# Optimization experiments

Hardware: AMD Instinct MI355X
Metric: run time of the kernel (lower is better)

## Reference

```python
import jax, jax.numpy as jnp
import numpy as np

N_CHANNELS = 32
DIM_CAPSULE = 16


def setup_inputs() -> dict:
    key = jax.random.key(0)
    k1, k2, k3 = jax.random.split(key, 3)
    B, H, W, Cin = 32, 56, 56, 256
    d, n = DIM_CAPSULE, N_CHANNELS
    inputs = jax.random.normal(k1, (B, H, W, Cin), dtype=jnp.float32)
    # glorot-ish scale for the 3x3 conv kernel
    convW_1 = jax.random.normal(k2, (3, 3, Cin, d * n), dtype=jnp.float32) * 0.02
    bias_1 = jnp.zeros((d * n,), dtype=jnp.float32)
    CapsAct_W = jax.random.normal(k3, (1, 1, d, d * n), dtype=jnp.float32) * 0.1
    CapsAct_B = jnp.zeros((d * n,), dtype=jnp.float32)
    return {"inputs": inputs, "convW_1": convW_1, "bias_1": bias_1,
            "CapsAct_W": CapsAct_W, "CapsAct_B": CapsAct_B}


def reference(inputs, convW_1, bias_1, CapsAct_W, CapsAct_B):
    d, n = DIM_CAPSULE, N_CHANNELS
    # 3x3 stride-2 SAME conv (NHWC / HWIO), bias, relu
    y = jax.lax.conv_general_dilated(
        inputs, convW_1, window_strides=(2, 2), padding="SAME",
        dimension_numbers=("NHWC", "HWIO", "NHWC"))
    y = jax.nn.relu(y + bias_1)                      # [B, Ho, Wo, d*n]
    B, Ho, Wo, _ = y.shape
    # Per-channel 1x1 convs == grouped matmul over capsule channels.
    yg = y.reshape(B, Ho, Wo, n, d)                  # group channels: [B,Ho,Wo,n,d_in]
    Wg = CapsAct_W.reshape(d, n, d)                  # [d_in, n, d_out]
    bg = CapsAct_B.reshape(n, d)                     # [n, d_out]
    # output layout matches tf: [B, Ho, Wo, dim_capsule, n_channels]
    out = jnp.einsum("bhwnd,dne->bhwen", yg, Wg) + bg.T[None, None, None]
    return out
```

## Files before the change

kernel.cpp:

```cpp
#include <hip/hip_runtime.h>
#include <hip/hip_bf16.h>

typedef __attribute__((ext_vector_type(4))) float f32x4;
typedef __attribute__((ext_vector_type(8))) short s16x8;
typedef __attribute__((ext_vector_type(8))) unsigned short u16x8;
typedef __attribute__((ext_vector_type(4))) unsigned short u16x4;

__device__ __forceinline__ unsigned short bfbits(float f) {
  unsigned int u = __builtin_bit_cast(unsigned int, f);
  return (unsigned short)((u + 0x8000u) >> 16);
}

__device__ __forceinline__ void gll16(void* lds, const void* g) {
  __builtin_amdgcn_global_load_lds(
      (const __attribute__((address_space(1))) unsigned int*)g,
      (__attribute__((address_space(3))) unsigned int*)lds, 16, 0, 0);
}

__global__ void prep_weights(const float* __restrict__ w,
                             __hip_bfloat16* __restrict__ wt) {
  int u = blockIdx.x * 256 + threadIdx.x;
  int n = u & 511;
  int c8 = (u >> 9) & 31;
  int kpos = u >> 14;
  int t = kpos * 8 + (c8 >> 2);
  int cq = c8 & 3;
  const float* src = w + ((kpos * 256 + c8 * 8) * 512) + n;
  u16x8 d;
#pragma unroll
  for (int j = 0; j < 8; ++j) d[j] = bfbits(src[j * 512]);
  int nb = n >> 7, nl = n & 127;
  *reinterpret_cast<u16x8*>(wt + ((t * 4 + nb) * 4096 + cq * 1024 + nl * 8)) = d;
}

__global__ __launch_bounds__(256)
void prep_input_t(const float* __restrict__ in, __hip_bfloat16* __restrict__ dst) {
  __shared__ __align__(16) unsigned short row[14848];
  int bh = blockIdx.x;
  int h = bh % 57, b = bh / 57;
  int t = threadIdx.x;
  __hip_bfloat16* d = (__hip_bfloat16*)dst + (long)bh * 14848;
  if (h < 56) {
    if (t < 64) {
      int par = t >> 5, cq = t & 31;
      u16x4 z = {0, 0, 0, 0};
      *(u16x4*)(row + (par * 32 + cq) * 232 + 224) = z;
      *(u16x4*)(row + (par * 32 + cq) * 232 + 228) = z;
    }
    const float* src = in + (long)(b * 56 + h) * 56 * 256;
#pragma unroll
    for (int j = 0; j < 14; ++j) {
      int idx = j * 256 + t;
      f32x4 v = *(const f32x4*)(src + idx * 4);
      int e0 = idx * 4;
      int w = e0 >> 8, c = e0 & 255;
      int off = ((w & 1) * 32 + (c >> 3)) * 232 + (w >> 1) * 8 + (c & 7);
      u16x4 q = {bfbits(v[0]), bfbits(v[1]), bfbits(v[2]), bfbits(v[3])};
      *(u16x4*)(row + off) = q;
    }
    __syncthreads();
    for (int i = t; i < 1856; i += 256)
      *(u16x8*)(d + i * 8) = *(const u16x8*)(row + i * 8);
  } else {
    u16x8 z = {0, 0, 0, 0, 0, 0, 0, 0};
    for (int i = t; i < 1856; i += 256) *(u16x8*)(d + i * 8) = z;
  }
}

__global__ __launch_bounds__(512, 4)
void caps_main_fast(const __hip_bfloat16* __restrict__ inp,
                    const __hip_bfloat16* __restrict__ wt,
                    const float* __restrict__ bias1,
                    const float* __restrict__ capsW,
                    const float* __restrict__ capsB,
                    float* __restrict__ out) {
  __shared__ __align__(16) unsigned char smem[73728];

  int bid = (int)blockIdx.x;
  bid = (bid & 7) * 49 + (bid >> 3);
  int mblk = bid >> 2;
  int nb = bid & 3;
  int p0 = mblk * 256;

  int tid = threadIdx.x;
  int lane = tid & 63;
  int wv = tid >> 6;
  int wm = (wv >> 1) * 64;
  int wn = (wv & 1) * 64;
  int col = lane & 15;
  int lq = lane >> 4;

  int mq = wv >> 1;
  int cqa = (wv & 1) * 2;
  int bcq = wv >> 1;
  int bnh = wv & 1;

  int p = p0 + mq * 64 + lane;
  int b = p / 784;
  int rr = p - b * 784;
  int ho = rr / 28;
  int wo = rr - ho * 28;
  int base0 = b * 846336 + 2 * ho * 14848 + wo * 8;

  const __hip_bfloat16* wtb = wt + nb * 4096;

  f32x4 acc[4][4] = {};

  auto stage = [&](int buf, int t) {
    int kp = t >> 3, tc = t & 7;
    int kh = (kp * 11) >> 5;
    int kw = kp - kh * 3;
    __hip_bfloat16* sa = (__hip_bfloat16*)smem + buf * 12288;
    __hip_bfloat16* sb = sa + 8192;
    const __hip_bfloat16* as =
        inp + base0 + kh * 14848 + (kw & 1) * 7424 + (kw >> 1) * 8 + (tc * 4 + cqa) * 232;
    gll16(sa + cqa * 2048 + mq * 512, as);
    gll16(sa + (cqa + 1) * 2048 + mq * 512, as + 232);
    const __hip_bfloat16* bs = wtb + t * 16384 + bcq * 1024 + bnh * 512 + lane * 8;
    gll16(sb + bcq * 1024 + bnh * 512, bs);
  };

  stage(0, 0);
  stage(1, 1);
  __asm__ volatile("s_waitcnt vmcnt(3)" ::: "memory");
  __builtin_amdgcn_s_barrier();

  int rd = 0;
  for (int t = 0; t < 72; ++t) {
    const __hip_bfloat16* sa = (const __hip_bfloat16*)smem + rd * 12288;
    const __hip_bfloat16* sb = sa + 8192;
    s16x8 af[4], bfr[4];
#pragma unroll
    for (int mf = 0; mf < 4; ++mf)
      af[mf] = *(const s16x8*)(sa + lq * 2048 + (wm + 16 * mf + col) * 8);
#pragma unroll
    for (int nf = 0; nf < 4; ++nf)
      bfr[nf] = *(const s16x8*)(sb + lq * 1024 + (wn + 16 * nf + col) * 8);
    if (t + 2 < 72) {
      int st = rd + 2; if (st >= 3) st -= 3;
      stage(st, t + 2);
    }
#pragma unroll
    for (int mf = 0; mf < 4; ++mf)
#pragma unroll
      for (int nf = 0; nf < 4; ++nf)
        acc[mf][nf] = __builtin_amdgcn_mfma_f32_16x16x32_bf16(
            af[mf], bfr[nf], acc[mf][nf], 0, 0, 0);
    if (t < 70) {
      __asm__ volatile("s_waitcnt vmcnt(3)" ::: "memory");
    } else {
      __asm__ volatile("s_waitcnt vmcnt(0)" ::: "memory");
    }
    __builtin_amdgcn_s_barrier();
    rd = (rd + 1 == 3) ? 0 : rd + 1;
  }

  __hip_bfloat16* yw = (__hip_bfloat16*)smem + wv * 4096;
  int nBase = nb * 128 + wn;
#pragma unroll
  for (int nf = 0; nf < 4; ++nf) {
    float b1v = bias1[nBase + nf * 16 + col];
#pragma unroll
    for (int mf = 0; mf < 4; ++mf) {
      f32x4 a = acc[mf][nf];
#pragma unroll
      for (int r = 0; r < 4; ++r) {
        int pl = mf * 16 + lq * 4 + r;
        int nl = nf * 16 + col;
        float v = a[r] + b1v;
        v = v > 0.f ? v : 0.f;
        int off = (pl * 128 + nl * 2) ^ ((pl & 7) << 4);
        *(unsigned short*)((char*)yw + off) = bfbits(v);
      }
    }
  }

  int gb = nb * 8 + (wv & 1) * 4;
  s16x8 wf[4];
  f32x4 cinit[4];
#pragma unroll
  for (int g = 0; g < 4; ++g) {
    int gg = gb + g;
    s16x8 bw = {0, 0, 0, 0, 0, 0, 0, 0};
    if (lq < 2) {
#pragma unroll
      for (int j = 0; j < 8; ++j)
        bw[j] = (short)bfbits(capsW[(8 * lq + j) * 512 + gg * 16 + col]);
    }
    wf[g] = bw;
    float cb = capsB[gg * 16 + col];
    cinit[g] = f32x4{cb, cb, cb, cb};
  }
#pragma unroll
  for (int mf = 0; mf < 4; ++mf) {
    int prow = 16 * mf + col;
    f32x4 dd[4];
#pragma unroll
    for (int g = 0; g < 4; ++g) {
      s16x8 afv = {0, 0, 0, 0, 0, 0, 0, 0};
      if (lq < 2) {
        int off = (prow * 128 + g * 32 + lq * 16) ^ ((prow & 7) << 4);
        afv = *(const s16x8*)((char*)yw + off);
      }
      dd[g] = __builtin_amdgcn_mfma_f32_16x16x32_bf16(afv, wf[g], cinit[g], 0, 0, 0);
    }
    long pgl = (long)(p0 + wm) + 16 * mf;
#pragma unroll
    for (int r = 0; r < 4; ++r) {
      long pg = pgl + 4 * lq + r;
      f32x4 o = {dd[0][r], dd[1][r], dd[2][r], dd[3][r]};
      *(f32x4*)(out + (pg * 16 + col) * 32 + gb) = o;
    }
  }
}

__global__ __launch_bounds__(256, 3)
void caps_main_v1(const float* __restrict__ in, const __hip_bfloat16* __restrict__ wt,
                  const float* __restrict__ bias1, const float* __restrict__ capsW,
                  const float* __restrict__ capsB, float* __restrict__ out) {
  __shared__ __align__(16) unsigned char smem[32768];
  __hip_bfloat16* sA = (__hip_bfloat16*)smem;
  __hip_bfloat16* sB = (__hip_bfloat16*)(smem + 8192);

  int bid = (int)blockIdx.x;
  bid = (bid & 7) * 98 + (bid >> 3);
  int mblk = bid >> 2;
  int nb = bid & 3;
  int p0 = mblk * 128;

  int tid = threadIdx.x;
  int lane = tid & 63;
  int wv = tid >> 6;
  int wm = (wv >> 1) * 64;
  int wn = (wv & 1) * 64;
  int col = lane & 15;
  int lq = lane >> 4;

  int am = tid & 127;
  int ah = tid >> 7;
  int p = p0 + am;
  int bb = p / 784;
  int rr = p - bb * 784;
  int ho = rr / 28;
  int wo = rr - ho * 28;

  f32x4 acc[4][4] = {};
  const __hip_bfloat16* wtb = wt + nb * 4096;

  for (int kp = 0; kp < 9; ++kp) {
    int kh = kp / 3;
    int kw = kp - kh * 3;
    int h = 2 * ho + kh, ww = 2 * wo + kw;
    bool valid = (h < 56) && (ww < 56);
    const float* arow = in + (((bb * 56 + h) * 56 + ww) * 256) + ah * 16;
#pragma unroll
    for (int tc = 0; tc < 8; ++tc) {
      int t = kp * 8 + tc;
      __syncthreads();
      const __hip_bfloat16* bsrc = wtb + t * 16384 + tid * 8;
      gll16(sB + (wv * 512), bsrc);
      gll16(sB + 2048 + (wv * 512), bsrc + 2048);
      f32x4 v0, v1, v2, v3;
      if (valid) {
        const f32x4* apv = (const f32x4*)(arow + tc * 32);
        v0 = apv[0]; v1 = apv[1]; v2 = apv[2]; v3 = apv[3];
      } else {
        v0 = f32x4{0.f, 0.f, 0.f, 0.f}; v1 = v0; v2 = v0; v3 = v0;
      }
      u16x8 pk0, pk1;
#pragma unroll
      for (int j = 0; j < 4; ++j) {
        pk0[j] = bfbits(v0[j]); pk0[j + 4] = bfbits(v1[j]);
        pk1[j] = bfbits(v2[j]); pk1[j + 4] = bfbits(v3[j]);
      }
      *(u16x8*)(sA + (ah * 2) * 1024 + am * 8) = pk0;
      *(u16x8*)(sA + (ah * 2 + 1) * 1024 + am * 8) = pk1;
      __syncthreads();
      s16x8 af[4], bfr[4];
#pragma unroll
      for (int mf = 0; mf < 4; ++mf)
        af[mf] = *(const s16x8*)(sA + lq * 1024 + (wm + 16 * mf + col) * 8);
#pragma unroll
      for (int nf = 0; nf < 4; ++nf)
        bfr[nf] = *(const s16x8*)(sB + lq * 1024 + (wn + 16 * nf + col) * 8);
#pragma unroll
      for (int mf = 0; mf < 4; ++mf)
#pragma unroll
        for (int nf = 0; nf < 4; ++nf)
          acc[mf][nf] = __builtin_amdgcn_mfma_f32_16x16x32_bf16(
              af[mf], bfr[nf], acc[mf][nf], 0, 0, 0);
    }
  }

  __syncthreads();

  __hip_bfloat16* yw = (__hip_bfloat16*)smem + wv * 4096;
  int nBase = nb * 128 + wn;
#pragma unroll
  for (int nf = 0; nf < 4; ++nf) {
    float b1v = bias1[nBase + nf * 16 + col];
#pragma unroll
    for (int mf = 0; mf < 4; ++mf) {
      f32x4 a = acc[mf][nf];
#pragma unroll
      for (int r = 0; r < 4; ++r) {
        int pl = mf * 16 + lq * 4 + r;
        int nl = nf * 16 + col;
        float v = a[r] + b1v;
        v = v > 0.f ? v : 0.f;
        int off = (pl * 128 + nl * 2) ^ ((pl & 7) << 4);
        *(unsigned short*)((char*)yw + off) = bfbits(v);
      }
    }
  }

  int gb = nb * 8 + (wv & 1) * 4;
  s16x8 wf[4];
  f32x4 cinit[4];
#pragma unroll
  for (int g = 0; g < 4; ++g) {
    int gg = gb + g;
    s16x8 bw = {0, 0, 0, 0, 0, 0, 0, 0};
    if (lq < 2) {
#pragma unroll
      for (int j = 0; j < 8; ++j)
        bw[j] = (short)bfbits(capsW[(8 * lq + j) * 512 + gg * 16 + col]);
    }
    wf[g] = bw;
    float cb = capsB[gg * 16 + col];
    cinit[g] = f32x4{cb, cb, cb, cb};
  }
#pragma unroll
  for (int mf = 0; mf < 4; ++mf) {
    int prow = 16 * mf + col;
    f32x4 dd[4];
#pragma unroll
    for (int g = 0; g < 4; ++g) {
      s16x8 afv = {0, 0, 0, 0, 0, 0, 0, 0};
      if (lq < 2) {
        int off = (prow * 128 + g * 32 + lq * 16) ^ ((prow & 7) << 4);
        afv = *(const s16x8*)((char*)yw + off);
      }
      dd[g] = __builtin_amdgcn_mfma_f32_16x16x32_bf16(afv, wf[g], cinit[g], 0, 0, 0);
    }
    long pgl = (long)(p0 + wm) + 16 * mf;
#pragma unroll
    for (int r = 0; r < 4; ++r) {
      long pg = pgl + 4 * lq + r;
      f32x4 o = {dd[0][r], dd[1][r], dd[2][r], dd[3][r]};
      *(f32x4*)(out + (pg * 16 + col) * 32 + gb) = o;
    }
  }
}

extern "C" void kernel_launch(void* const* d_in, const int* in_sizes, int n_in,
                              void* d_out, int out_size, void* d_ws, size_t ws_size,
                              hipStream_t stream) {
  const float* inputs = (const float*)d_in[0];
  const float* convW  = (const float*)d_in[1];
  const float* bias1  = (const float*)d_in[2];
  const float* capsW  = (const float*)d_in[3];
  const float* capsB  = (const float*)d_in[4];
  float* out = (float*)d_out;

  __hip_bfloat16* wt = (__hip_bfloat16*)d_ws;
  const size_t IN_OFF = 2621440;
  const size_t NEED = IN_OFF + (size_t)27082752 * 2;

  prep_weights<<<576, 256, 0, stream>>>(convW, wt);
  if (ws_size >= NEED) {
    __hip_bfloat16* inp = (__hip_bfloat16*)((char*)d_ws + IN_OFF);
    prep_input_t<<<1824, 256, 0, stream>>>(inputs, inp);
    caps_main_fast<<<392, 512, 0, stream>>>(inp, wt, bias1, capsW, capsB, out);
  } else {
    caps_main_v1<<<784, 256, 0, stream>>>(inputs, wt, bias1, capsW, capsB, out);
  }
}
```

Baseline: 109.7 us.

## Load conv A fragments directly from global and merge prep kernels

The main conv loop stops staging the input (A) tiles through LDS and has each wave read its A fragments straight from global memory into registers. Only the weight (B) tile still goes through LDS, now double-buffered, and the MFMA block is raised in priority with setprio. The two prep kernels are merged into one launch to cut launch overhead, and the LDS footprint shrinks. The risks are exposed global latency on A, because those loads are used in the same iteration without prefetch, and duplicate A loads across waves. The fallback path also writes the converted input into a workspace that is too small for it.

After: 108.9 us. Within noise of the previous version (-0.7%).

```diff
diff --git a/kernel.cpp b/kernel.cpp
--- a/kernel.cpp
+++ b/kernel.cpp
@@ -17,53 +17,53 @@
       (__attribute__((address_space(3))) unsigned int*)lds, 16, 0, 0);
 }
 
-__global__ void prep_weights(const float* __restrict__ w,
-                             __hip_bfloat16* __restrict__ wt) {
-  int u = blockIdx.x * 256 + threadIdx.x;
-  int n = u & 511;
-  int c8 = (u >> 9) & 31;
-  int kpos = u >> 14;
-  int t = kpos * 8 + (c8 >> 2);
-  int cq = c8 & 3;
-  const float* src = w + ((kpos * 256 + c8 * 8) * 512) + n;
-  u16x8 d;
-#pragma unroll
-  for (int j = 0; j < 8; ++j) d[j] = bfbits(src[j * 512]);
-  int nb = n >> 7, nl = n & 127;
-  *reinterpret_cast<u16x8*>(wt + ((t * 4 + nb) * 4096 + cq * 1024 + nl * 8)) = d;
-}
-
 __global__ __launch_bounds__(256)
-void prep_input_t(const float* __restrict__ in, __hip_bfloat16* __restrict__ dst) {
-  __shared__ __align__(16) unsigned short row[14848];
-  int bh = blockIdx.x;
-  int h = bh % 57, b = bh / 57;
+void prep_all(const float* __restrict__ in, __hip_bfloat16* __restrict__ dst,
+              const float* __restrict__ w, __hip_bfloat16* __restrict__ wt) {
   int t = threadIdx.x;
-  __hip_bfloat16* d = (__hip_bfloat16*)dst + (long)bh * 14848;
-  if (h < 56) {
-    if (t < 64) {
-      int par = t >> 5, cq = t & 31;
-      u16x4 z = {0, 0, 0, 0};
-      *(u16x4*)(row + (par * 32 + cq) * 232 + 224) = z;
-      *(u16x4*)(row + (par * 32 + cq) * 232 + 228) = z;
-    }
-    const float* src = in + (long)(b * 56 + h) * 56 * 256;
-#pragma unroll
-    for (int j = 0; j < 14; ++j) {
-      int idx = j * 256 + t;
-      f32x4 v = *(const f32x4*)(src + idx * 4);
-      int e0 = idx * 4;
-      int w = e0 >> 8, c = e0 & 255;
-      int off = ((w & 1) * 32 + (c >> 3)) * 232 + (w >> 1) * 8 + (c & 7);
-      u16x4 q = {bfbits(v[0]), bfbits(v[1]), bfbits(v[2]), bfbits(v[3])};
-      *(u16x4*)(row + off) = q;
-    }
-    __syncthreads();
-    for (int i = t; i < 1856; i += 256)
-      *(u16x8*)(d + i * 8) = *(const u16x8*)(row + i * 8);
+  if (blockIdx.x < 1824) {
+    __shared__ __align__(16) unsigned short row[14848];
+    int bh = blockIdx.x;
+    int h = bh % 57, b = bh / 57;
+    __hip_bfloat16* d = (__hip_bfloat16*)dst + (long)bh * 14848;
+    if (h < 56) {
+      if (t < 64) {
+        int par = t >> 5, cq = t & 31;
+        u16x4 z = {0, 0, 0, 0};
+        *(u16x4*)(row + (par * 32 + cq) * 232 + 224) = z;
+        *(u16x4*)(row + (par * 32 + cq) * 232 + 228) = z;
+      }
+      const float* src = in + (long)(b * 56 + h) * 56 * 256;
+#pragma unroll
+      for (int j = 0; j < 14; ++j) {
+        int idx = j * 256 + t;
+        f32x4 v = *(const f32x4*)(src + idx * 4);
+        int e0 = idx * 4;
+        int ww = e0 >> 8, c = e0 & 255;
+        int off = ((ww & 1) * 32 + (c >> 3)) * 232 + (ww >> 1) * 8 + (c & 7);
+        u16x4 q = {bfbits(v[0]), bfbits(v[1]), bfbits(v[2]), bfbits(v[3])};
+        *(u16x4*)(row + off) = q;
+      }
+      __syncthreads();
+      for (int i = t; i < 1856; i += 256)
+        *(u16x8*)(d + i * 8) = *(const u16x8*)(row + i * 8);
+    } else {
+      u16x8 z = {0, 0, 0, 0, 0, 0, 0, 0};
+      for (int i = t; i < 1856; i += 256) *(u16x8*)(d + i * 8) = z;
+    }
   } else {
-    u16x8 z = {0, 0, 0, 0, 0, 0, 0, 0};
-    for (int i = t; i < 1856; i += 256) *(u16x8*)(d + i * 8) = z;
+    int u = (blockIdx.x - 1824) * 256 + t;
+    int n = u & 511;
+    int c8 = (u >> 9) & 31;
+    int kpos = u >> 14;
+    int tt = kpos * 8 + (c8 >> 2);
+    int cq = c8 & 3;
+    const float* src = w + ((kpos * 256 + c8 * 8) * 512) + n;
+    u16x8 d;
+#pragma unroll
+    for (int j = 0; j < 8; ++j) d[j] = bfbits(src[j * 512]);
+    int nb = n >> 7, nl = n & 127;
+    *reinterpret_cast<u16x8*>(wt + ((tt * 4 + nb) * 4096 + cq * 1024 + nl * 8)) = d;
   }
 }
 
@@ -74,7 +74,8 @@
                     const float* __restrict__ capsW,
                     const float* __restrict__ capsB,
                     float* __restrict__ out) {
-  __shared__ __align__(16) unsigned char smem[73728];
+  __shared__ __align__(16) unsigned char smem[65536];
+  __hip_bfloat16* smem_e = (__hip_bfloat16*)smem;
 
   int bid = (int)blockIdx.x;
   bid = (bid & 7) * 49 + (bid >> 3);
@@ -90,89 +91,60 @@
   int col = lane & 15;
   int lq = lane >> 4;
 
-  int mq = wv >> 1;
-  int cqa = (wv & 1) * 2;
   int bcq = wv >> 1;
   int bnh = wv & 1;
-
-  int p = p0 + mq * 64 + lane;
-  int b = p / 784;
-  int rr = p - b * 784;
-  int ho = rr / 28;
-  int wo = rr - ho * 28;
-  int base0 = b * 846336 + 2 * ho * 14848 + wo * 8;
+  int ldsB = bcq * 1024 + bnh * 512;
+
+  int baseAf[4];
+#pragma unroll
+  for (int mf = 0; mf < 4; ++mf) {
+    int pA = p0 + wm + 16 * mf + col;
+    int bb = pA / 784, rA = pA - bb * 784;
+    int hA = rA / 28, wA = rA - hA * 28;
+    baseAf[mf] = bb * 846336 + 2 * hA * 14848 + wA * 8 + lq * 232;
+  }
 
   const __hip_bfloat16* wtb = wt + nb * 4096;
+  const __hip_bfloat16* bsrc = wtb + bcq * 1024 + bnh * 512 + lane * 8;
 
   f32x4 acc[4][4] = {};
 
-  auto stage = [&](int buf, int t) {
+  gll16(smem_e + ldsB, bsrc);
+  __asm__ volatile("s_waitcnt vmcnt(0)" ::: "memory");
+  __builtin_amdgcn_s_barrier();
+  __asm__ volatile("" ::: "memory");
+
+  int buf = 0;
+  for (int t = 0; t < 72; ++t) {
     int kp = t >> 3, tc = t & 7;
     int kh = (kp * 11) >> 5;
     int kw = kp - kh * 3;
-    __hip_bfloat16* sa = (__hip_bfloat16*)smem + buf * 12288;
-    __hip_bfloat16* sb = sa + 8192;
-    const __hip_bfloat16* as =
-        inp + base0 + kh * 14848 + (kw & 1) * 7424 + (kw >> 1) * 8 + (tc * 4 + cqa) * 232;
-    gll16(sa + cqa * 2048 + mq * 512, as);
-    gll16(sa + (cqa + 1) * 2048 + mq * 512, as + 232);
-    const __hip_bfloat16* bs = wtb + t * 16384 + bcq * 1024 + bnh * 512 + lane * 8;
-    gll16(sb + bcq * 1024 + bnh * 512, bs);
-  };
-
-  stage(0, 0);
-  stage(1, 1);
-  __asm__ volatile("s_waitcnt vmcnt(3)" ::: "memory");
-  __builtin_amdgcn_s_barrier();
-
-  int rd = 0;
-  for (int t = 0; t < 72; ++t) {
-    const __hip_bfloat16* sa = (const __hip_bfloat16*)smem + rd * 12288;
-    const __hip_bfloat16* sb = sa + 8192;
-    s16x8 af[4], bfr[4];
+    int koff = kh * 14848 + (kw & 1) * 7424 + (kw >> 1) * 8 + tc * 928;
+    s16x8 af[4];
 #pragma unroll
     for (int mf = 0; mf < 4; ++mf)
-      af[mf] = *(const s16x8*)(sa + lq * 2048 + (wm + 16 * mf + col) * 8);
+      af[mf] = *(const s16x8*)(inp + baseAf[mf] + koff);
+    const __hip_bfloat16* sb = smem_e + buf * 4096;
+    s16x8 bq[4];
 #pragma unroll
     for (int nf = 0; nf < 4; ++nf)
-      bfr[nf] = *(const s16x8*)(sb + lq * 1024 + (wn + 16 * nf + col) * 8);
-    if (t + 2 < 72) {
-      int st = rd + 2; if (st >= 3) st -= 3;
-      stage(st, t + 2);
-    }
+      bq[nf] = *(const s16x8*)(sb + lq * 1024 + (wn + 16 * nf + col) * 8);
+    if (t < 71)
+      gll16(smem_e + (buf ^ 1) * 4096 + ldsB, bsrc + (t + 1) * 16384);
+    __builtin_amdgcn_s_setprio(1);
 #pragma unroll
     for (int mf = 0; mf < 4; ++mf)
 #pragma unroll
       for (int nf = 0; nf < 4; ++nf)
         acc[mf][nf] = __builtin_amdgcn_mfma_f32_16x16x32_bf16(
-            af[mf], bfr[nf], acc[mf][nf], 0, 0, 0);
-    if (t < 70) {
-      __asm__ volatile("s_waitcnt vmcnt(3)" ::: "memory");
-    } else {
+            af[mf], bq[nf], acc[mf][nf], 0, 0, 0);
+    __builtin_amdgcn_s_setprio(0);
+    if (t < 71) {
       __asm__ volatile("s_waitcnt vmcnt(0)" ::: "memory");
-    }
-    __builtin_amdgcn_s_barrier();
-    rd = (rd + 1 == 3) ? 0 : rd + 1;
-  }
-
-  __hip_bfloat16* yw = (__hip_bfloat16*)smem + wv * 4096;
-  int nBase = nb * 128 + wn;
-#pragma unroll
-  for (int nf = 0; nf < 4; ++nf) {
-    float b1v = bias1[nBase + nf * 16 + col];
-#pragma unroll
-    for (int mf = 0; mf < 4; ++mf) {
-      f32x4 a = acc[mf][nf];
-#pragma unroll
-      for (int r = 0; r < 4; ++r) {
-        int pl = mf * 16 + lq * 4 + r;
-        int nl = nf * 16 + col;
-        float v = a[r] + b1v;
-        v = v > 0.f ? v : 0.f;
-        int off = (pl * 128 + nl * 2) ^ ((pl & 7) << 4);
-        *(unsigned short*)((char*)yw + off) = bfbits(v);
-      }
-    }
+      __builtin_amdgcn_s_barrier();
+      __asm__ volatile("" ::: "memory");
+    }
+    buf ^= 1;
   }
 
   int gb = nb * 8 + (wv & 1) * 4;
@@ -191,6 +163,33 @@
     float cb = capsB[gg * 16 + col];
     cinit[g] = f32x4{cb, cb, cb, cb};
   }
+  float b1v[4];
+  int nBase = nb * 128 + wn;
+#pragma unroll
+  for (int nf = 0; nf < 4; ++nf) b1v[nf] = bias1[nBase + nf * 16 + col];
+
+  __asm__ volatile("s_waitcnt vmcnt(0) lgkmcnt(0)" ::: "memory");
+  __builtin_amdgcn_s_barrier();
+  __asm__ volatile("" ::: "memory");
+
+  __hip_bfloat16* yw = smem_e + wv * 4096;
+#pragma unroll
+  for (int nf = 0; nf < 4; ++nf) {
+#pragma unroll
+    for (int mf = 0; mf < 4; ++mf) {
+      f32x4 a = acc[mf][nf];
+#pragma unroll
+      for (int r = 0; r < 4; ++r) {
+        int pl = mf * 16 + lq * 4 + r;
+        int nl = nf * 16 + col;
+        float v = a[r] + b1v[nf];
+        v = v > 0.f ? v : 0.f;
+        int off = (pl * 128 + nl * 2) ^ ((pl & 7) << 4);
+        *(unsigned short*)((char*)yw + off) = bfbits(v);
+      }
+    }
+  }
+
 #pragma unroll
   for (int mf = 0; mf < 4; ++mf) {
     int prow = 16 * mf + col;
@@ -367,12 +366,12 @@
   const size_t IN_OFF = 2621440;
   const size_t NEED = IN_OFF + (size_t)27082752 * 2;
 
-  prep_weights<<<576, 256, 0, stream>>>(convW, wt);
   if (ws_size >= NEED) {
     __hip_bfloat16* inp = (__hip_bfloat16*)((char*)d_ws + IN_OFF);
-    prep_input_t<<<1824, 256, 0, stream>>>(inputs, inp);
+    prep_all<<<2400, 256, 0, stream>>>(inputs, inp, convW, wt);
     caps_main_fast<<<392, 512, 0, stream>>>(inp, wt, bias1, capsW, capsB, out);
   } else {
+    prep_all<<<2400, 256, 0, stream>>>(inputs, (__hip_bfloat16*)d_ws, convW, wt);
     caps_main_v1<<<784, 256, 0, stream>>>(inputs, wt, bias1, capsW, capsB, out);
   }
 }
```
